# Optimization experiments

Measured on AMD Instinct MI355X. Metric: run time of the kernel, lower is better.

The kernel has to match this reference:

```python
import jax, jax.numpy as jnp
import numpy as np

DIM = 3072
KV_DIM = 2048
HEADS = 16
DIM_HEAD = 128
INNER = HEADS * DIM_HEAD  # 2048
EPS = 1e-5


def layer_norm(x, g, b):
    mu = jnp.mean(x, axis=-1, keepdims=True)
    var = jnp.var(x, axis=-1, keepdims=True)
    return (x - mu) * jax.lax.rsqrt(var + EPS) * g + b


def setup_inputs() -> dict:
    key = jax.random.key(0)
    ks = jax.random.split(key, 8)
    b, n1, n2 = 2, 2048, 2048
    x = jax.random.normal(ks[0], (b, n1, KV_DIM), dtype=jnp.float32)
    latents = jax.random.normal(ks[1], (b, n2, DIM), dtype=jnp.float32)
    w_q = jax.random.normal(ks[2], (DIM, INNER), dtype=jnp.float32) / np.sqrt(DIM)
    w_kv = jax.random.normal(ks[3], (KV_DIM, 2 * INNER), dtype=jnp.float32) / np.sqrt(KV_DIM)
    w_out = jax.random.normal(ks[4], (INNER, DIM), dtype=jnp.float32) / np.sqrt(INNER)
    ln1_g = jnp.ones((KV_DIM,), jnp.float32)
    ln1_b = jnp.zeros((KV_DIM,), jnp.float32)
    ln2_g = jnp.ones((DIM,), jnp.float32)
    ln2_b = jnp.zeros((DIM,), jnp.float32)
    return {"x": x, "latents": latents, "w_q": w_q, "w_kv": w_kv,
            "w_out": w_out, "ln1_g": ln1_g, "ln1_b": ln1_b,
            "ln2_g": ln2_g, "ln2_b": ln2_b}


def reference(x, latents, w_q, w_kv, w_out, ln1_g, ln1_b, ln2_g, ln2_b):
    b, n2, _ = latents.shape
    xn = layer_norm(x, ln1_g, ln1_b)            # (b, n1, kv_dim)
    ln = layer_norm(latents, ln2_g, ln2_b)      # (b, n2, dim)
    q = ln @ w_q                                # (b, n2, inner)
    kv = xn @ w_kv                              # (b, n1, 2*inner)
    k, v = jnp.split(kv, 2, axis=-1)
    # (b, h, n, d)
    def split_heads(t):
        bs, n, _ = t.shape
        return t.reshape(bs, n, HEADS, DIM_HEAD).transpose(0, 2, 1, 3)
    q, k, v = split_heads(q), split_heads(k), split_heads(v)
    scale = 1.0 / np.sqrt(np.sqrt(DIM_HEAD)).astype(np.float32)
    w = jnp.einsum('bhqd,bhkd->bhqk', q * scale, k * scale)
    w = jax.nn.softmax(w.astype(jnp.float32), axis=-1).astype(q.dtype)
    out = jnp.einsum('bhqk,bhkd->bhqd', w, v)
    out = out.transpose(0, 2, 1, 3).reshape(b, n2, INNER)
    return out @ w_out
```

## Files before the change

kernel.cpp:

```cpp
#include <hip/hip_runtime.h>
#include <type_traits>


using u16 = unsigned short;
using u32 = unsigned int;
typedef __attribute__((ext_vector_type(8))) short short8;
typedef __attribute__((ext_vector_type(4))) float floatx4;

typedef __attribute__((address_space(1))) const unsigned int gu32;
typedef __attribute__((address_space(3))) unsigned int lu32;

__device__ __forceinline__ void gld16(void* lds, const void* g) {
  __builtin_amdgcn_global_load_lds((gu32*)g, (lu32*)lds, 16, 0, 0);
}

__device__ inline u16 f2bf(float f) {
  u32 u = __float_as_uint(f);
  u32 r = (u + 0x7FFFu + ((u >> 16) & 1u)) >> 16;
  return (u16)r;
}

template <int L>
__global__ __launch_bounds__(256) void ln_cast(const float* __restrict__ in,
                                               const float* __restrict__ gw,
                                               const float* __restrict__ bw,
                                               u16* __restrict__ out) {
  constexpr int C4 = L / 1024;
  const int row = blockIdx.x;
  const int t = threadIdx.x;
  const float* rp = in + (size_t)row * L;
  float4 v[C4];
  float s = 0.f, ss = 0.f;
#pragma unroll
  for (int c = 0; c < C4; ++c) {
    v[c] = *(const float4*)(rp + (c * 256 + t) * 4);
    s += v[c].x + v[c].y + v[c].z + v[c].w;
    ss += v[c].x * v[c].x + v[c].y * v[c].y + v[c].z * v[c].z + v[c].w * v[c].w;
  }
#pragma unroll
  for (int off = 32; off > 0; off >>= 1) {
    s += __shfl_down(s, off);
    ss += __shfl_down(ss, off);
  }
  __shared__ float red[8];
  const int wave = t >> 6, lane = t & 63;
  if (lane == 0) { red[wave] = s; red[4 + wave] = ss; }
  __syncthreads();
  const float tot = red[0] + red[1] + red[2] + red[3];
  const float tss = red[4] + red[5] + red[6] + red[7];
  const float mu = tot * (1.f / L);
  const float rstd = rsqrtf(tss * (1.f / L) - mu * mu + 1e-5f);
  u16* op = out + (size_t)row * L;
#pragma unroll
  for (int c = 0; c < C4; ++c) {
    const int base = (c * 256 + t) * 4;
    float4 gv = *(const float4*)(gw + base);
    float4 bv = *(const float4*)(bw + base);
    u32 p0 = (u32)f2bf((v[c].x - mu) * rstd * gv.x + bv.x) |
             ((u32)f2bf((v[c].y - mu) * rstd * gv.y + bv.y) << 16);
    u32 p1 = (u32)f2bf((v[c].z - mu) * rstd * gv.z + bv.z) |
             ((u32)f2bf((v[c].w - mu) * rstd * gv.w + bv.w) << 16);
    uint2 pk; pk.x = p0; pk.y = p1;
    *(uint2*)(op + base) = pk;
  }
}

__global__ __launch_bounds__(256) void transpose_cast(const float* __restrict__ in,
                                                      u16* __restrict__ out,
                                                      int R, int C) {
  __shared__ u16 tile[32][33];
  const int c0 = blockIdx.x * 32, r0 = blockIdx.y * 32;
  const int x = threadIdx.x, y = threadIdx.y;
#pragma unroll
  for (int j = 0; j < 4; ++j)
    tile[y + 8 * j][x] = f2bf(in[(size_t)(r0 + y + 8 * j) * C + c0 + x]);
  __syncthreads();
#pragma unroll
  for (int j = 0; j < 4; ++j)
    out[(size_t)(c0 + y + 8 * j) * R + r0 + x] = tile[x][y + 8 * j];
}

__global__ __launch_bounds__(256) void transpose_v(const u16* __restrict__ kvb,
                                                   u16* __restrict__ vT) {
  __shared__ u16 tile[32][33];
  const int bh = blockIdx.z, b = bh >> 4, h = bh & 15;
  const u16* src = kvb + (size_t)b * 2048 * 4096 + 2048 + h * 128;
  u16* dst = vT + (size_t)bh * 128 * 2048;
  const int d0 = blockIdx.x * 32, n0 = blockIdx.y * 32;
  const int x = threadIdx.x, y = threadIdx.y;
#pragma unroll
  for (int j = 0; j < 4; ++j)
    tile[y + 8 * j][x] = src[(size_t)(n0 + y + 8 * j) * 4096 + d0 + x];
  __syncthreads();
#pragma unroll
  for (int j = 0; j < 4; ++j)
    dst[(size_t)(d0 + y + 8 * j) * 2048 + n0 + x] = tile[x][y + 8 * j];
}

template <typename OutT>
__global__ __launch_bounds__(256) void gemm_bt(const u16* __restrict__ A,
                                               const u16* __restrict__ Bt,
                                               OutT* __restrict__ C,
                                               int M, int N, int K) {
  __shared__ u16 As[128 * 64];
  __shared__ u16 Bs[128 * 64];
  const int tid = threadIdx.x;
  const int wave = tid >> 6, lane = tid & 63, l16 = lane & 15, quad = lane >> 4;
  const int wm = (wave >> 1) * 64, wn = (wave & 1) * 64;
  const long m0 = (long)blockIdx.y * 128, n0 = (long)blockIdx.x * 128;
  const int srow = tid >> 3;
  const int gc = ((tid & 7) ^ ((tid >> 3) & 7)) * 8;
  const u16* Ag0 = A + (m0 + srow) * (long)K + gc;
  const u16* Bg0 = Bt + (n0 + srow) * (long)K + gc;
  const long rowoff = 32L * K;

  const floatx4 fz = {0.f, 0.f, 0.f, 0.f};
  floatx4 acc[4][4];
#pragma unroll
  for (int i = 0; i < 4; ++i)
#pragma unroll
    for (int j = 0; j < 4; ++j) acc[i][j] = fz;

  for (int k0 = 0; k0 < K; k0 += 64) {
    __syncthreads();
#pragma unroll
    for (int c = 0; c < 4; ++c) {
      gld16(&As[(c * 256 + tid) * 8], Ag0 + c * rowoff + k0);
      gld16(&Bs[(c * 256 + tid) * 8], Bg0 + c * rowoff + k0);
    }
    __syncthreads();
#pragma unroll
    for (int kd = 0; kd < 2; ++kd) {
      const int sw = ((4 * kd + quad) ^ (l16 & 7)) * 8;
      short8 a[4], b[4];
#pragma unroll
      for (int i = 0; i < 4; ++i) a[i] = *(const short8*)&As[(wm + i * 16 + l16) * 64 + sw];
#pragma unroll
      for (int j = 0; j < 4; ++j) b[j] = *(const short8*)&Bs[(wn + j * 16 + l16) * 64 + sw];
#pragma unroll
      for (int i = 0; i < 4; ++i)
#pragma unroll
        for (int j = 0; j < 4; ++j)
          acc[i][j] = __builtin_amdgcn_mfma_f32_16x16x32_bf16(a[i], b[j], acc[i][j], 0, 0, 0);
    }
  }

#pragma unroll
  for (int i = 0; i < 4; ++i)
#pragma unroll
    for (int r = 0; r < 4; ++r) {
      const long row = m0 + wm + i * 16 + quad * 4 + r;
#pragma unroll
      for (int j = 0; j < 4; ++j) {
        const long col = n0 + wn + j * 16 + l16;
        if constexpr (std::is_same<OutT, float>::value)
          C[row * N + col] = acc[i][j][r];
        else
          C[row * N + col] = f2bf(acc[i][j][r]);
      }
    }
}

__global__ __launch_bounds__(256, 2) void flash_attn(const u16* __restrict__ Q,
                                                     const u16* __restrict__ KV,
                                                     const u16* __restrict__ VT,
                                                     u16* __restrict__ O) {
  __shared__ u16 Ks[2][64 * 128];
  __shared__ u16 Vs[2][128 * 64];
  __shared__ u16 Ps[4][32 * 64];
  const int tid = threadIdx.x;
  const int wave = tid >> 6, lane = tid & 63, l16 = lane & 15, quad = lane >> 4;
  const int d = blockIdx.x;
  const int bh = (d & 7) * 4 + ((d >> 3) & 3);
  const int qt = d >> 5;
  const int b = bh >> 4, h = bh & 15;
  const u16* Qb = Q + (size_t)b * 2048 * 2048 + h * 128;
  const u16* Kb = KV + (size_t)b * 2048 * 4096 + h * 128;
  const u16* Vb = VT + (size_t)bh * 128 * 2048;
  u16* Ob = O + (size_t)b * 2048 * 2048 + h * 128;
  const int q0 = qt * 128 + wave * 32;

  short8 qf[2][4];
#pragma unroll
  for (int t = 0; t < 2; ++t)
#pragma unroll
    for (int kd = 0; kd < 4; ++kd)
      qf[t][kd] = *(const short8*)&Qb[(size_t)(q0 + t * 16 + l16) * 2048 + kd * 32 + quad * 8];

  short8 onesf;
  {
    union { short8 s; u32 w[4]; } uo;
    const u32 o = (l16 == 0) ? 0x3F803F80u : 0u;
#pragma unroll
    for (int i = 0; i < 4; ++i) uo.w[i] = o;
    onesf = uo.s;
  }

  const floatx4 fz = {0.f, 0.f, 0.f, 0.f};
  floatx4 oacc[2][9];
  float m[2][4];
#pragma unroll
  for (int t = 0; t < 2; ++t) {
#pragma unroll
    for (int jd = 0; jd < 9; ++jd) oacc[t][jd] = fz;
#pragma unroll
    for (int r = 0; r < 4; ++r) m[t][r] = -1e30f;
  }

  u16* Psw = Ps[wave];
  const float sc2 = 0.12751775f;
  const float THR2 = 11.5416f;

  auto stage = [&](int buf, int kv0) {
#pragma unroll
    for (int c = 0; c < 4; ++c) {
      const int li = c * 256 + tid;
      const int krow = li >> 4, kdb = (li & 15) ^ (krow & 15);
      gld16(&Ks[buf][li * 8], Kb + (size_t)(kv0 + krow) * 4096 + kdb * 8);
      const int vrow = li >> 3, vdb = (li & 7) ^ (vrow & 7);
      gld16(&Vs[buf][li * 8], Vb + (size_t)vrow * 2048 + kv0 + vdb * 8);
    }
  };

  stage(0, 0);
  int cur = 0;

  for (int kt = 0; kt < 32; ++kt) {
    __syncthreads();
    if (kt < 31) stage(cur ^ 1, (kt + 1) * 64);
    const u16* Kc = Ks[cur];
    const u16* Vc = Vs[cur];

    floatx4 sacc[2][4];
#pragma unroll
    for (int t = 0; t < 2; ++t)
#pragma unroll
      for (int jn = 0; jn < 4; ++jn) sacc[t][jn] = fz;
    __builtin_amdgcn_s_setprio(1);
#pragma unroll
    for (int jn = 0; jn < 4; ++jn)
#pragma unroll
      for (int kd = 0; kd < 4; ++kd) {
        short8 kb = *(const short8*)&Kc[(jn * 16 + l16) * 128 + ((4 * kd + quad) ^ l16) * 8];
        sacc[0][jn] = __builtin_amdgcn_mfma_f32_16x16x32_bf16(qf[0][kd], kb, sacc[0][jn], 0, 0, 0);
        sacc[1][jn] = __builtin_amdgcn_mfma_f32_16x16x32_bf16(qf[1][kd], kb, sacc[1][jn], 0, 0, 0);
      }
    __builtin_amdgcn_s_setprio(0);

#pragma unroll
    for (int t = 0; t < 2; ++t) {
#pragma unroll
      for (int r = 0; r < 4; ++r) {
        float mx = fmaxf(fmaxf(sacc[t][0][r], sacc[t][1][r]),
                         fmaxf(sacc[t][2][r], sacc[t][3][r]));
#pragma unroll
        for (int off = 8; off > 0; off >>= 1) mx = fmaxf(mx, __shfl_xor(mx, off, 16));
        const float mxs = sc2 * mx;
        if (!__all(mxs - m[t][r] <= THR2)) {
          const float mnew = fmaxf(m[t][r], mxs);
          const float alpha = __builtin_amdgcn_exp2f(m[t][r] - mnew);
          m[t][r] = mnew;
#pragma unroll
          for (int jd = 0; jd < 9; ++jd) oacc[t][jd][r] *= alpha;
        }
        const float mrow = m[t][r];
        const int q = t * 16 + quad * 4 + r;
        const int mask = (q & 7) ^ (q >> 3);
        u16* prow = &Psw[q * 64 + (l16 & 7)];
#pragma unroll
        for (int jn = 0; jn < 4; ++jn) {
          const float p = __builtin_amdgcn_exp2f(fmaf(sc2, sacc[t][jn][r], -mrow));
          const int slot = (2 * jn + (l16 >> 3)) ^ mask;
          prow[slot * 8] = f2bf(p);
        }
      }
    }

    const int pmask0 = (l16 & 7) ^ (l16 >> 3);
    const int pmask1 = (l16 & 7) ^ (2 + (l16 >> 3));
    __builtin_amdgcn_s_setprio(1);
#pragma unroll
    for (int kk = 0; kk < 2; ++kk) {
      const int chunk = 4 * kk + quad;
      short8 pf0 = *(const short8*)&Psw[(l16) * 64 + (chunk ^ pmask0) * 8];
      short8 pf1 = *(const short8*)&Psw[(16 + l16) * 64 + (chunk ^ pmask1) * 8];
#pragma unroll
      for (int jd = 0; jd < 8; ++jd) {
        short8 vb = *(const short8*)&Vc[(jd * 16 + l16) * 64 + (chunk ^ (l16 & 7)) * 8];
        oacc[0][jd] = __builtin_amdgcn_mfma_f32_16x16x32_bf16(pf0, vb, oacc[0][jd], 0, 0, 0);
        oacc[1][jd] = __builtin_amdgcn_mfma_f32_16x16x32_bf16(pf1, vb, oacc[1][jd], 0, 0, 0);
      }
      oacc[0][8] = __builtin_amdgcn_mfma_f32_16x16x32_bf16(pf0, onesf, oacc[0][8], 0, 0, 0);
      oacc[1][8] = __builtin_amdgcn_mfma_f32_16x16x32_bf16(pf1, onesf, oacc[1][8], 0, 0, 0);
    }
    __builtin_amdgcn_s_setprio(0);
    cur ^= 1;
  }

#pragma unroll
  for (int t = 0; t < 2; ++t)
#pragma unroll
    for (int r = 0; r < 4; ++r) {
      const float l = __shfl(oacc[t][8][r], lane & 48);
      const float inv = 1.f / l;
      const size_t row = q0 + t * 16 + quad * 4 + r;
#pragma unroll
      for (int jd = 0; jd < 8; ++jd)
        Ob[row * 2048 + jd * 16 + l16] = f2bf(oacc[t][jd][r] * inv);
    }
}

extern "C" void kernel_launch(void* const* d_in, const int* in_sizes, int n_in,
                              void* d_out, int out_size, void* d_ws, size_t ws_size,
                              hipStream_t stream) {
  const float* x       = (const float*)d_in[0];
  const float* latents = (const float*)d_in[1];
  const float* w_q     = (const float*)d_in[2];
  const float* w_kv    = (const float*)d_in[3];
  const float* w_out   = (const float*)d_in[4];
  const float* ln1_g   = (const float*)d_in[5];
  const float* ln1_b   = (const float*)d_in[6];
  const float* ln2_g   = (const float*)d_in[7];
  const float* ln2_b   = (const float*)d_in[8];

  char* ws = (char*)d_ws;
  u16* xn    = (u16*)(ws);
  u16* lnl   = (u16*)(ws + 16777216);
  u16* wqT   = (u16*)(ws + 41943040);
  u16* wkvT  = (u16*)(ws + 54525952);
  u16* woutT = (u16*)(ws + 71303168);
  u16* qb    = (u16*)(ws + 83886080);
  u16* kvb   = (u16*)(ws + 100663296);
  u16* vTb   = lnl;
  u16* attn  = xn;

  ln_cast<2048><<<dim3(4096), 256, 0, stream>>>(x, ln1_g, ln1_b, xn);
  ln_cast<3072><<<dim3(4096), 256, 0, stream>>>(latents, ln2_g, ln2_b, lnl);

  transpose_cast<<<dim3(64, 96), dim3(32, 8), 0, stream>>>(w_q, wqT, 3072, 2048);
  transpose_cast<<<dim3(128, 64), dim3(32, 8), 0, stream>>>(w_kv, wkvT, 2048, 4096);
  transpose_cast<<<dim3(96, 64), dim3(32, 8), 0, stream>>>(w_out, woutT, 2048, 3072);

  gemm_bt<u16><<<dim3(16, 32), 256, 0, stream>>>(lnl, wqT, qb, 4096, 2048, 3072);
  gemm_bt<u16><<<dim3(32, 32), 256, 0, stream>>>(xn, wkvT, kvb, 4096, 4096, 2048);

  transpose_v<<<dim3(4, 64, 32), dim3(32, 8), 0, stream>>>(kvb, vTb);

  flash_attn<<<dim3(512), 256, 0, stream>>>(qb, kvb, vTb, attn);

  gemm_bt<float><<<dim3(24, 32), 256, 0, stream>>>(attn, woutT, (float*)d_out, 4096, 3072, 2048);
}
```

Measured before the change: 548.7 us.

## Add 256x256-tile 8-wave GEMM with staged quadrant pipeline for KV and output projections

Adds a new GEMM kernel with 256x256 output tiles, 512 threads and double-buffered LDS filled by direct global-to-LDS loads. The main loop is split into four quadrant phases that interleave prefetch of the next K slice with MFMA work, using explicit waitcnt, barriers and setprio. It replaces the 128x128 GEMM for the KV projection and the output projection to raise data reuse per tile. The cost is far fewer workgroups (256 and 192) on a many-CU device, which may leave CUs idle, plus 128 KB of LDS per block.

```diff
diff --git a/kernel.cpp b/kernel.cpp
--- a/kernel.cpp
+++ b/kernel.cpp
@@ -160,6 +160,150 @@
       }
     }
 }
+
+#define GBAR()                                         \
+  do {                                                 \
+    asm volatile("" ::: "memory");                     \
+    __builtin_amdgcn_s_barrier();                      \
+    asm volatile("" ::: "memory");                     \
+  } while (0)
+#define VMW(N) asm volatile("s_waitcnt vmcnt(" #N ")" ::: "memory")
+
+#define G8_LDA(MH)                                                             \
+  {                                                                            \
+    const u16* Ab_ = &As[buf][(MH) * 8192 + (wr * 32 + l16) * 64];             \
+    _Pragma("unroll") for (int mi = 0; mi < 2; ++mi)                           \
+    _Pragma("unroll") for (int ks = 0; ks < 2; ++ks)                           \
+      af[mi][ks] = *(const short8*)&Ab_[mi * 1024 + ((4 * ks + quad) ^ swz) * 8]; \
+  }
+#define G8_LDB(DST, NH)                                                        \
+  {                                                                            \
+    const u16* Bb_ = &Bs[buf][(NH) * 8192 + (wc * 64 + l16) * 64];             \
+    _Pragma("unroll") for (int ni = 0; ni < 4; ++ni)                           \
+    _Pragma("unroll") for (int ks = 0; ks < 2; ++ks)                           \
+      DST[ni][ks] = *(const short8*)&Bb_[ni * 1024 + ((4 * ks + quad) ^ swz) * 8]; \
+  }
+#define G8_MFMA(MH, BFX, NH)                                                   \
+  __builtin_amdgcn_s_setprio(1);                                               \
+  _Pragma("unroll") for (int ks = 0; ks < 2; ++ks)                             \
+  _Pragma("unroll") for (int mi = 0; mi < 2; ++mi)                             \
+  _Pragma("unroll") for (int ni = 0; ni < 4; ++ni)                             \
+    acc[MH][mi][NH][ni] = __builtin_amdgcn_mfma_f32_16x16x32_bf16(             \
+        af[mi][ks], BFX[ni][ks], acc[MH][mi][NH][ni], 0, 0, 0);                \
+  __builtin_amdgcn_s_setprio(0);
+
+template <typename OutT>
+__global__ __launch_bounds__(512, 2) void gemm_bt8(const u16* __restrict__ A,
+                                                   const u16* __restrict__ Bt,
+                                                   OutT* __restrict__ C,
+                                                   int M, int N, int K) {
+  __shared__ u16 As[2][16384];
+  __shared__ u16 Bs[2][16384];
+  (void)M;
+  const int tid = threadIdx.x;
+  const int wave = tid >> 6, lane = tid & 63, l16 = lane & 15, quad = lane >> 4;
+  const int wr = wave >> 1;
+  const int wc = wave & 1;
+  const int nwg = gridDim.x * gridDim.y;
+  const int bid0 = blockIdx.y * gridDim.x + blockIdx.x;
+  const int bid = (bid0 & 7) * (nwg >> 3) + (bid0 >> 3);
+  const int bx = bid % gridDim.x, by = bid / gridDim.x;
+  const long m0 = (long)by * 256, n0 = (long)bx * 256;
+
+  const int srow = tid >> 3;
+  const int gc = ((tid & 7) ^ (srow & 7)) * 8;
+
+  auto stageA = [&](int bufn, int h, int k0) {
+#pragma unroll
+    for (int c = 0; c < 2; ++c)
+      gld16(&As[bufn][h * 8192 + (c * 512 + tid) * 8],
+            A + (size_t)(m0 + h * 128 + c * 64 + srow) * K + k0 + gc);
+  };
+  auto stageB = [&](int bufn, int h, int k0) {
+#pragma unroll
+    for (int c = 0; c < 2; ++c)
+      gld16(&Bs[bufn][h * 8192 + (c * 512 + tid) * 8],
+            Bt + (size_t)(n0 + h * 128 + c * 64 + srow) * K + k0 + gc);
+  };
+
+  const floatx4 fz = {0.f, 0.f, 0.f, 0.f};
+  floatx4 acc[2][2][2][4];
+#pragma unroll
+  for (int a = 0; a < 2; ++a)
+#pragma unroll
+    for (int b = 0; b < 2; ++b)
+#pragma unroll
+      for (int c = 0; c < 2; ++c)
+#pragma unroll
+        for (int d = 0; d < 4; ++d) acc[a][b][c][d] = fz;
+
+  short8 af[2][2], bf0[4][2], bf1[4][2];
+  const int swz = l16 & 7;
+
+  stageA(0, 0, 0);
+  stageB(0, 0, 0);
+  stageB(0, 1, 0);
+  stageA(0, 1, 0);
+  VMW(4);
+  GBAR();
+
+  const int NT = K >> 6;
+  for (int t = 0; t < NT; ++t) {
+    const int buf = t & 1;
+    const int kn = (t + 1) << 6;
+    const bool pre = (t + 1 < NT);
+
+    G8_LDA(0);
+    G8_LDB(bf0, 0);
+    if (pre) stageA(buf ^ 1, 0, kn);
+    GBAR();
+    G8_MFMA(0, bf0, 0);
+    if (pre) { VMW(4); } else { VMW(2); }
+    GBAR();
+
+    G8_LDB(bf1, 1);
+    if (pre) stageB(buf ^ 1, 0, kn);
+    GBAR();
+    G8_MFMA(0, bf1, 1);
+    if (pre) { VMW(4); } else { VMW(0); }
+    GBAR();
+
+    G8_LDA(1);
+    if (pre) stageB(buf ^ 1, 1, kn);
+    GBAR();
+    G8_MFMA(1, bf0, 0);
+    GBAR();
+
+    if (pre) stageA(buf ^ 1, 1, kn);
+    GBAR();
+    G8_MFMA(1, bf1, 1);
+    if (pre) { VMW(4); }
+    GBAR();
+  }
+
+#pragma unroll
+  for (int mh = 0; mh < 2; ++mh)
+#pragma unroll
+    for (int mi = 0; mi < 2; ++mi)
+#pragma unroll
+      for (int rr = 0; rr < 4; ++rr) {
+        const long row = m0 + mh * 128 + wr * 32 + mi * 16 + quad * 4 + rr;
+#pragma unroll
+        for (int nh = 0; nh < 2; ++nh)
+#pragma unroll
+          for (int ni = 0; ni < 4; ++ni) {
+            const long col = n0 + nh * 128 + wc * 64 + ni * 16 + l16;
+            if constexpr (std::is_same<OutT, float>::value)
+              C[row * N + col] = acc[mh][mi][nh][ni][rr];
+            else
+              C[row * N + col] = f2bf(acc[mh][mi][nh][ni][rr]);
+          }
+      }
+}
+
+#undef G8_LDA
+#undef G8_LDB
+#undef G8_MFMA
 
 __global__ __launch_bounds__(256, 2) void flash_attn(const u16* __restrict__ Q,
                                                      const u16* __restrict__ KV,
@@ -342,11 +486,11 @@
   transpose_cast<<<dim3(96, 64), dim3(32, 8), 0, stream>>>(w_out, woutT, 2048, 3072);
 
   gemm_bt<u16><<<dim3(16, 32), 256, 0, stream>>>(lnl, wqT, qb, 4096, 2048, 3072);
-  gemm_bt<u16><<<dim3(32, 32), 256, 0, stream>>>(xn, wkvT, kvb, 4096, 4096, 2048);
+  gemm_bt8<u16><<<dim3(16, 16), 512, 0, stream>>>(xn, wkvT, kvb, 4096, 4096, 2048);
 
   transpose_v<<<dim3(4, 64, 32), dim3(32, 8), 0, stream>>>(kvb, vTb);
 
   flash_attn<<<dim3(512), 256, 0, stream>>>(qb, kvb, vTb, attn);
 
-  gemm_bt<float><<<dim3(24, 32), 256, 0, stream>>>(attn, woutT, (float*)d_out, 4096, 3072, 2048);
-}
+  gemm_bt8<float><<<dim3(12, 16), 512, 0, stream>>>(attn, woutT, (float*)d_out, 4096, 3072, 2048);
+}
```

New measurement: 513.3 us. -6.5%, faster.
